# Kernel optimization log

Hardware: AMD Instinct MI355X
Metric: run time of the kernel (lower is better)

## Reference

```python
import jax, jax.numpy as jnp
import numpy as np

UNITS = 256
NUM_HEADS = 8
HEAD_DIM = UNITS // NUM_HEADS
B, N = 8, 2048


def setup_inputs() -> dict:
    key = jax.random.key(0)
    ks = jax.random.split(key, 7)
    node_features = jax.random.normal(ks[0], (B, N, UNITS), dtype=jnp.float32)
    adjacency_matrix = jax.random.randint(ks[1], (B, N, N), 0, 2, dtype=jnp.int32)
    # Glorot-ish scaled dense weights
    s = 1.0 / np.sqrt(UNITS)
    Wq = jax.random.normal(ks[2], (UNITS, UNITS), dtype=jnp.float32) * s
    Wk = jax.random.normal(ks[3], (UNITS, UNITS), dtype=jnp.float32) * s
    Wv = jax.random.normal(ks[4], (UNITS, UNITS), dtype=jnp.float32) * s
    Wo = jax.random.normal(ks[5], (UNITS, UNITS), dtype=jnp.float32) * s
    bo = jnp.zeros((UNITS,), dtype=jnp.float32)
    return {"node_features": node_features, "adjacency_matrix": adjacency_matrix,
            "Wq": Wq, "Wk": Wk, "Wv": Wv, "Wo": Wo, "bo": bo}


def reference(node_features, adjacency_matrix, Wq, Wk, Wv, Wo, bo):
    b, n, _ = node_features.shape
    h, d = NUM_HEADS, HEAD_DIM
    # projections -> [b, h, n, d]
    q = (node_features @ Wq).reshape(b, n, h, d).transpose(0, 2, 1, 3)
    k = (node_features @ Wk).reshape(b, n, h, d).transpose(0, 2, 1, 3)
    v = (node_features @ Wv).reshape(b, n, h, d).transpose(0, 2, 1, 3)
    scores = jnp.einsum('bhqd,bhkd->bhqk', q, k) / jnp.sqrt(jnp.float32(d))
    mask = adjacency_matrix[:, None, :, :] > 0  # [b,1,n,n] broadcasts over heads
    scores = jnp.where(mask, scores, jnp.float32(-1e9))
    w = jax.nn.softmax(scores, axis=-1)
    # dropout is identity at inference (training=None)
    ctx = jnp.einsum('bhqk,bhkd->bhqd', w, v)
    ctx = ctx.transpose(0, 2, 1, 3).reshape(b, n, h * d)
    return ctx @ Wo + bo
```

## Files before the change

kernel.cpp:

```cpp
#include <hip/hip_runtime.h>
#include <cstdint>
#include <cstddef>

#define B_ 8
#define N_ 2048
#define H_ 8
#define D_ 32
#define U_ 256

typedef _Float16 half8 __attribute__((ext_vector_type(8)));
typedef _Float16 half4 __attribute__((ext_vector_type(4)));
typedef float float4v __attribute__((ext_vector_type(4)));

__device__ __forceinline__ float fast_exp2(float x) {
#if __has_builtin(__builtin_amdgcn_exp2f)
  return __builtin_amdgcn_exp2f(x);
#else
  return exp2f(x);
#endif
}

__global__ __launch_bounds__(256)
void k_prep(const float* __restrict__ X,
            const float* __restrict__ Wq, const float* __restrict__ Wk,
            const float* __restrict__ Wv, const float* __restrict__ Wo,
            _Float16* __restrict__ Xh, _Float16* __restrict__ WT)
{
  __shared__ __attribute__((aligned(16))) float Ts[64][68];
  const int tid = threadIdx.x;
  const int bx = blockIdx.x;
  if (bx < 4) {
    const float* W = (bx == 0) ? Wq : (bx == 1) ? Wk : (bx == 2) ? Wv : Wo;
    const float scale = (bx == 0) ? 0.25505413f : 1.0f;
    _Float16* dstW = WT + (size_t)bx * (U_ * U_);
    const int r = tid >> 2, cs = tid & 3;
    for (int t = 0; t < 16; ++t) {
      const int k0 = (t >> 2) * 64, n0 = (t & 3) * 64;
#pragma unroll
      for (int j = 0; j < 4; ++j)
        *(float4v*)&Ts[r][cs * 16 + j * 4] =
            *(const float4v*)(W + (size_t)(k0 + r) * U_ + n0 + cs * 16 + j * 4);
      __syncthreads();
#pragma unroll
      for (int j = 0; j < 4; ++j) {
        half4 hv;
#pragma unroll
        for (int jj = 0; jj < 4; ++jj)
          hv[jj] = (_Float16)(Ts[cs * 16 + j * 4 + jj][r] * scale);
        *(half4*)(dstW + (size_t)(n0 + r) * U_ + k0 + cs * 16 + j * 4) = hv;
      }
      __syncthreads();
    }
  } else {
    const size_t base = ((size_t)(bx - 4) * 256 + tid) * 32;
#pragma unroll
    for (int i = 0; i < 4; ++i) {
      float4v a  = *(const float4v*)(X + base + i * 8);
      float4v b2 = *(const float4v*)(X + base + i * 8 + 4);
      half8 hv;
      hv[0] = (_Float16)a[0];  hv[1] = (_Float16)a[1];
      hv[2] = (_Float16)a[2];  hv[3] = (_Float16)a[3];
      hv[4] = (_Float16)b2[0]; hv[5] = (_Float16)b2[1];
      hv[6] = (_Float16)b2[2]; hv[7] = (_Float16)b2[3];
      *(half8*)(Xh + base + i * 8) = hv;
    }
  }
}

__global__ __launch_bounds__(256, 2)
void k_qkv2(const _Float16* __restrict__ Xh,
            const _Float16* __restrict__ WTq, const _Float16* __restrict__ WTk,
            const _Float16* __restrict__ WTv,
            _Float16* __restrict__ Qg, _Float16* __restrict__ Kg,
            _Float16* __restrict__ VTg)
{
  __shared__ __attribute__((aligned(16))) char qsmem[36864];
  _Float16* Xs = (_Float16*)qsmem;
  _Float16* Ws = (_Float16*)(qsmem + 18432);

  const int tid  = threadIdx.x;
  const int lane = tid & 63;
  const int w    = tid >> 6;
  const int c    = lane & 15;
  const int qd   = lane >> 4;

  const int bx   = blockIdx.x;
  const int proj = bx >> 1;
  const int nh   = bx & 1;
  const int n0l  = nh * 128;
  const int m0   = blockIdx.y * 128;
  const _Float16* WT = (proj == 0) ? WTq : ((proj == 1) ? WTk : WTv);

  const float4v zero4 = {0.f, 0.f, 0.f, 0.f};
  float4v acc[2][8];
#pragma unroll
  for (int i = 0; i < 2; ++i)
#pragma unroll
    for (int j = 0; j < 8; ++j) acc[i][j] = zero4;

  const int row = tid >> 1;
  const int off = (tid & 1) * 32;
  for (int kt = 0; kt < 4; ++kt) {
    const int k0 = kt * 64;
    {
      const _Float16* src = Xh + (size_t)(m0 + row) * U_ + k0 + off;
      _Float16* dst = &Xs[row * 72 + off];
#pragma unroll
      for (int i = 0; i < 4; ++i)
        *(half8*)(dst + i * 8) = *(const half8*)(src + i * 8);
    }
    {
      const _Float16* srcw = WT + (size_t)(n0l + row) * U_ + k0 + off;
      _Float16* dstw = &Ws[row * 72 + off];
#pragma unroll
      for (int i = 0; i < 4; ++i)
        *(half8*)(dstw + i * 8) = *(const half8*)(srcw + i * 8);
    }
    __syncthreads();
#pragma unroll
    for (int ks = 0; ks < 2; ++ks) {
      half8 af[2], bf[8];
#pragma unroll
      for (int mt = 0; mt < 2; ++mt)
        af[mt] = *(const half8*)&Xs[(w * 32 + mt * 16 + c) * 72 + ks * 32 + qd * 8];
#pragma unroll
      for (int nt = 0; nt < 8; ++nt)
        bf[nt] = *(const half8*)&Ws[(nt * 16 + c) * 72 + ks * 32 + qd * 8];
#pragma unroll
      for (int mt = 0; mt < 2; ++mt)
#pragma unroll
        for (int nt = 0; nt < 8; ++nt)
          acc[mt][nt] = __builtin_amdgcn_mfma_f32_16x16x32_f16(af[mt], bf[nt], acc[mt][nt], 0, 0, 0);
    }
    __syncthreads();
  }

  const int b   = m0 >> 11;
  const int nb0 = m0 & (N_ - 1);
  if (proj < 2) {
    _Float16* Og = (proj == 0) ? Qg : Kg;
#pragma unroll
    for (int mt = 0; mt < 2; ++mt)
#pragma unroll
      for (int nt = 0; nt < 8; ++nt)
#pragma unroll
        for (int r = 0; r < 4; ++r) {
          const int rowl = w * 32 + mt * 16 + qd * 4 + r;
          Og[(size_t)(b * N_ + nb0 + rowl) * U_ + n0l + nt * 16 + c] = (_Float16)acc[mt][nt][r];
        }
  } else {
    _Float16* tr = (_Float16*)qsmem;
#pragma unroll
    for (int mt = 0; mt < 2; ++mt)
#pragma unroll
      for (int nt = 0; nt < 8; ++nt)
#pragma unroll
        for (int r = 0; r < 4; ++r)
          tr[(nt * 16 + c) * 136 + w * 32 + mt * 16 + qd * 4 + r] = (_Float16)acc[mt][nt][r];
    __syncthreads();
    const int u = tid >> 1;
    const int seg = tid & 1;
    _Float16* dst = VTg + (size_t)(b * U_ + n0l + u) * N_ + nb0 + seg * 64;
#pragma unroll
    for (int i = 0; i < 8; ++i)
      *(half8*)(dst + i * 8) = *(const half8*)&tr[u * 136 + seg * 64 + i * 8];
  }
}

__global__ __launch_bounds__(256, 2)
void k_qkv(const float* __restrict__ X,
           const float* __restrict__ Wq, const float* __restrict__ Wk,
           const float* __restrict__ Wv,
           _Float16* __restrict__ Qg, _Float16* __restrict__ Kg,
           _Float16* __restrict__ VTg)
{
  __shared__ __attribute__((aligned(16))) char qsmem[36864];
  _Float16* Xs = (_Float16*)qsmem;
  _Float16* Ws = (_Float16*)(qsmem + 18432);

  const int tid  = threadIdx.x;
  const int lane = tid & 63;
  const int w    = tid >> 6;
  const int c    = lane & 15;
  const int qd   = lane >> 4;

  const int bx   = blockIdx.x;
  const int proj = bx >> 1;
  const int nh   = bx & 1;
  const int n0l  = nh * 128;
  const int m0   = blockIdx.y * 128;
  const float* Wp = (proj == 0) ? Wq : ((proj == 1) ? Wk : Wv);
  const float wscale = (proj == 0) ? 0.25505413f : 1.0f;

  const float4v zero4 = {0.f, 0.f, 0.f, 0.f};
  float4v acc[2][8];
#pragma unroll
  for (int i = 0; i < 2; ++i)
#pragma unroll
    for (int j = 0; j < 8; ++j) acc[i][j] = zero4;

  for (int kt = 0; kt < 4; ++kt) {
    const int k0 = kt * 64;
    {
      const int row = tid >> 1;
      const int off = (tid & 1) * 32;
      const float* src = X + (size_t)(m0 + row) * U_ + k0 + off;
      _Float16* dst = &Xs[row * 72 + off];
#pragma unroll
      for (int i = 0; i < 4; ++i) {
        float4v a  = *(const float4v*)(src + i * 8);
        float4v b2 = *(const float4v*)(src + i * 8 + 4);
        half8 hv;
        hv[0] = (_Float16)a[0];  hv[1] = (_Float16)a[1];
        hv[2] = (_Float16)a[2];  hv[3] = (_Float16)a[3];
        hv[4] = (_Float16)b2[0]; hv[5] = (_Float16)b2[1];
        hv[6] = (_Float16)b2[2]; hv[7] = (_Float16)b2[3];
        *(half8*)(dst + i * 8) = hv;
      }
    }
    {
      const int kl = tid & 63;
      const int ng = tid >> 6;
      const float* srcw = Wp + (size_t)(k0 + kl) * U_ + n0l + ng * 32;
#pragma unroll
      for (int j = 0; j < 8; ++j) {
        float4v a = *(const float4v*)(srcw + j * 4);
#pragma unroll
        for (int jj = 0; jj < 4; ++jj)
          Ws[(ng * 32 + j * 4 + jj) * 72 + kl] = (_Float16)(a[jj] * wscale);
      }
    }
    __syncthreads();
#pragma unroll
    for (int ks = 0; ks < 2; ++ks) {
      half8 af[2], bf[8];
#pragma unroll
      for (int mt = 0; mt < 2; ++mt)
        af[mt] = *(const half8*)&Xs[(w * 32 + mt * 16 + c) * 72 + ks * 32 + qd * 8];
#pragma unroll
      for (int nt = 0; nt < 8; ++nt)
        bf[nt] = *(const half8*)&Ws[(nt * 16 + c) * 72 + ks * 32 + qd * 8];
#pragma unroll
      for (int mt = 0; mt < 2; ++mt)
#pragma unroll
        for (int nt = 0; nt < 8; ++nt)
          acc[mt][nt] = __builtin_amdgcn_mfma_f32_16x16x32_f16(af[mt], bf[nt], acc[mt][nt], 0, 0, 0);
    }
    __syncthreads();
  }

  const int b   = m0 >> 11;
  const int nb0 = m0 & (N_ - 1);
  if (proj < 2) {
    _Float16* Og = (proj == 0) ? Qg : Kg;
#pragma unroll
    for (int mt = 0; mt < 2; ++mt)
#pragma unroll
      for (int nt = 0; nt < 8; ++nt)
#pragma unroll
        for (int r = 0; r < 4; ++r) {
          const int rowl = w * 32 + mt * 16 + qd * 4 + r;
          Og[(size_t)(b * N_ + nb0 + rowl) * U_ + n0l + nt * 16 + c] = (_Float16)acc[mt][nt][r];
        }
  } else {
    _Float16* tr = (_Float16*)qsmem;
#pragma unroll
    for (int mt = 0; mt < 2; ++mt)
#pragma unroll
      for (int nt = 0; nt < 8; ++nt)
#pragma unroll
        for (int r = 0; r < 4; ++r)
          tr[(nt * 16 + c) * 136 + w * 32 + mt * 16 + qd * 4 + r] = (_Float16)acc[mt][nt][r];
    __syncthreads();
    const int u = tid >> 1;
    const int seg = tid & 1;
    _Float16* dst = VTg + (size_t)(b * U_ + n0l + u) * N_ + nb0 + seg * 64;
#pragma unroll
    for (int i = 0; i < 8; ++i)
      *(half8*)(dst + i * 8) = *(const half8*)&tr[u * 136 + seg * 64 + i * 8];
  }
}

#define KS_H (32 * 264)
#define VT_H (256 * 40)

struct StageRegs {
  half8 k0, v0;
  int a0, a1;
};

__global__ __launch_bounds__(1024, 4)
void k_attn(const _Float16* __restrict__ Qg, const _Float16* __restrict__ Kg,
            const _Float16* __restrict__ VTg, const int* __restrict__ Adj,
            _Float16* __restrict__ Cg)
{
  __shared__ __attribute__((aligned(16))) _Float16 KsB[2][KS_H];
  __shared__ __attribute__((aligned(16))) _Float16 VTsB[2][VT_H];
  __shared__ __attribute__((aligned(8)))  unsigned int maskB[2][64];

  const int tid  = threadIdx.x;
  const int lane = tid & 63;
  const int w    = tid >> 6;
  const int h    = w & 7;
  const int qh   = w >> 3;
  const int c    = lane & 15;
  const int qd   = lane >> 4;
  const int wg   = blockIdx.x;
  const int b    = wg & 7;
  const int q0   = (wg >> 3) * 64;

  const _Float16* kptr = Kg + (size_t)(b * N_ + (tid >> 5)) * U_ + (tid & 31) * 8;
  const _Float16* vptr = VTg + (size_t)(b * U_ + (tid >> 2)) * N_ + (tid & 3) * 8;
  const int rr = lane >> 5;
  const int kk = lane & 31;
  const int* aptr = Adj + (size_t)(b * N_ + q0 + w * 4 + rr) * N_ + kk;

  half8 qb[2];
#pragma unroll
  for (int nt = 0; nt < 2; ++nt)
    qb[nt] = *(const half8*)(Qg + (size_t)(b * N_ + q0 + qh * 32 + nt * 16 + c) * U_ + h * D_ + qd * 8);

  const float4v init4 = {-8.f, -8.f, -8.f, -8.f};
  const float4v zero4 = {0.f, 0.f, 0.f, 0.f};
  float4v acc[2][2];
#pragma unroll
  for (int i = 0; i < 2; ++i)
#pragma unroll
    for (int j = 0; j < 2; ++j) acc[i][j] = zero4;
  float lrow[2] = {0.f, 0.f};

  auto load_tile = [&](int kt) -> StageRegs {
    StageRegs r;
    r.k0 = *(const half8*)(kptr + (size_t)kt * 32 * U_);
    r.v0 = *(const half8*)(vptr + (size_t)kt * 32);
    const int* as = aptr + (size_t)kt * 32;
    r.a0 = as[0];
    r.a1 = as[2 * N_];
    return r;
  };
  auto store_tile = [&](const StageRegs& r, int buf) {
    *(half8*)&KsB[buf][(tid >> 5) * 264 + (tid & 31) * 8] = r.k0;
    *(half8*)&VTsB[buf][(tid >> 2) * 40 + (tid & 3) * 8] = r.v0;
    unsigned long long bm;
    bm = __ballot(r.a0 > 0); if (lane == 0) *(unsigned long long*)&maskB[buf][w * 4 + 0] = bm;
    bm = __ballot(r.a1 > 0); if (lane == 0) *(unsigned long long*)&maskB[buf][w * 4 + 2] = bm;
  };
  auto compute_tile = [&](int buf) {
    half8 ka0 = *(const half8*)&KsB[buf][(0 * 16 + c) * 264 + h * D_ + qd * 8];
    half8 ka1 = *(const half8*)&KsB[buf][(1 * 16 + c) * 264 + h * D_ + qd * 8];
    half4 va[2][2];
#pragma unroll
    for (int mt = 0; mt < 2; ++mt)
#pragma unroll
      for (int kc = 0; kc < 2; ++kc)
        va[mt][kc] = *(const half4*)&VTsB[buf][(h * D_ + mt * 16 + c) * 40 + kc * 16 + qd * 4];
#pragma unroll
    for (int nt = 0; nt < 2; ++nt) {
      float4v s0 = __builtin_amdgcn_mfma_f32_16x16x32_f16(ka0, qb[nt], init4, 0, 0, 0);
      float4v s1 = __builtin_amdgcn_mfma_f32_16x16x32_f16(ka1, qb[nt], init4, 0, 0, 0);
      const unsigned int mq = maskB[buf][qh * 32 + nt * 16 + c];
      const unsigned int t0 = mq >> (qd * 4);
      const unsigned int t1 = mq >> (16 + qd * 4);
      half4 pb0, pb1;
      float ls = 0.f;
#pragma unroll
      for (int r = 0; r < 4; ++r) {
        float e0 = fast_exp2(s0[r]);
        float e1 = fast_exp2(s1[r]);
        float p0 = ((t0 >> r) & 1u) ? e0 : 0.f;
        float p1 = ((t1 >> r) & 1u) ? e1 : 0.f;
        ls += p0 + p1;
        pb0[r] = (_Float16)p0;
        pb1[r] = (_Float16)p1;
      }
      lrow[nt] += ls;
      acc[0][nt] = __builtin_amdgcn_mfma_f32_16x16x16f16(va[0][0], pb0, acc[0][nt], 0, 0, 0);
      acc[0][nt] = __builtin_amdgcn_mfma_f32_16x16x16f16(va[0][1], pb1, acc[0][nt], 0, 0, 0);
      acc[1][nt] = __builtin_amdgcn_mfma_f32_16x16x16f16(va[1][0], pb0, acc[1][nt], 0, 0, 0);
      acc[1][nt] = __builtin_amdgcn_mfma_f32_16x16x16f16(va[1][1], pb1, acc[1][nt], 0, 0, 0);
    }
  };

  StageRegs rA = load_tile(0);
  store_tile(rA, 0);
  StageRegs rB = load_tile(1);
  __syncthreads();

#pragma unroll 1
  for (int kt = 0; kt < 64; kt += 2) {
    if (kt + 2 < 64) rA = load_tile(kt + 2);
    compute_tile(0);
    store_tile(rB, 1);
    __syncthreads();
    if (kt + 3 < 64) rB = load_tile(kt + 3);
    compute_tile(1);
    if (kt + 2 < 64) store_tile(rA, 0);
    __syncthreads();
  }

  float rinv[2];
#pragma unroll
  for (int nt = 0; nt < 2; ++nt) {
    float l = lrow[nt];
    l += __shfl_xor(l, 16, 64);
    l += __shfl_xor(l, 32, 64);
    rinv[nt] = (l > 0.f) ? 1.f / l : 0.f;
  }
  _Float16* ctxS = (_Float16*)KsB;
#pragma unroll
  for (int mt = 0; mt < 2; ++mt)
#pragma unroll
    for (int nt = 0; nt < 2; ++nt) {
      half4 hv;
#pragma unroll
      for (int r = 0; r < 4; ++r)
        hv[r] = (_Float16)(acc[mt][nt][r] * rinv[nt]);
      *(half4*)&ctxS[(qh * 32 + nt * 16 + c) * 264 + h * D_ + mt * 16 + qd * 4] = hv;
    }
  __syncthreads();
  {
    const int row = tid >> 4;
    const int seg = tid & 15;
    _Float16* dst = Cg + (size_t)(b * N_ + q0 + row) * U_ + seg * 16;
    *(half8*)(dst + 0) = *(const half8*)&ctxS[row * 264 + seg * 16];
    *(half8*)(dst + 8) = *(const half8*)&ctxS[row * 264 + seg * 16 + 8];
  }
}

__global__ __launch_bounds__(256, 2)
void k_out2(const _Float16* __restrict__ Cg, const _Float16* __restrict__ WTo,
            const float* __restrict__ bo, float* __restrict__ Out)
{
  __shared__ __attribute__((aligned(16))) char osmem[36864];
  _Float16* Xs = (_Float16*)osmem;
  _Float16* Ws = (_Float16*)(osmem + 18432);

  const int tid  = threadIdx.x;
  const int lane = tid & 63;
  const int w    = tid >> 6;
  const int c    = lane & 15;
  const int qd   = lane >> 4;
  const int n0l  = blockIdx.x * 128;
  const int m0   = blockIdx.y * 128;

  const float4v zero4 = {0.f, 0.f, 0.f, 0.f};
  float4v acc[2][8];
#pragma unroll
  for (int i = 0; i < 2; ++i)
#pragma unroll
    for (int j = 0; j < 8; ++j) acc[i][j] = zero4;

  const int row = tid >> 1;
  const int off = (tid & 1) * 32;
  for (int kt = 0; kt < 4; ++kt) {
    const int k0 = kt * 64;
    {
      const _Float16* src = Cg + (size_t)(m0 + row) * U_ + k0 + off;
      _Float16* dst = &Xs[row * 72 + off];
#pragma unroll
      for (int i = 0; i < 4; ++i)
        *(half8*)(dst + i * 8) = *(const half8*)(src + i * 8);
    }
    {
      const _Float16* srcw = WTo + (size_t)(n0l + row) * U_ + k0 + off;
      _Float16* dstw = &Ws[row * 72 + off];
#pragma unroll
      for (int i = 0; i < 4; ++i)
        *(half8*)(dstw + i * 8) = *(const half8*)(srcw + i * 8);
    }
    __syncthreads();
#pragma unroll
    for (int ks = 0; ks < 2; ++ks) {
      half8 af[2], bf[8];
#pragma unroll
      for (int mt = 0; mt < 2; ++mt)
        af[mt] = *(const half8*)&Xs[(w * 32 + mt * 16 + c) * 72 + ks * 32 + qd * 8];
#pragma unroll
      for (int nt = 0; nt < 8; ++nt)
        bf[nt] = *(const half8*)&Ws[(nt * 16 + c) * 72 + ks * 32 + qd * 8];
#pragma unroll
      for (int mt = 0; mt < 2; ++mt)
#pragma unroll
        for (int nt = 0; nt < 8; ++nt)
          acc[mt][nt] = __builtin_amdgcn_mfma_f32_16x16x32_f16(af[mt], bf[nt], acc[mt][nt], 0, 0, 0);
    }
    __syncthreads();
  }

#pragma unroll
  for (int nt = 0; nt < 8; ++nt) {
    const float bias = bo[n0l + nt * 16 + c];
#pragma unroll
    for (int mt = 0; mt < 2; ++mt)
#pragma unroll
      for (int r = 0; r < 4; ++r) {
        const int rowl = w * 32 + mt * 16 + qd * 4 + r;
        Out[(size_t)(m0 + rowl) * U_ + n0l + nt * 16 + c] = acc[mt][nt][r] + bias;
      }
  }
}

__global__ __launch_bounds__(256, 2)
void k_out(const _Float16* __restrict__ Cg, const float* __restrict__ Wo,
           const float* __restrict__ bo, float* __restrict__ Out)
{
  __shared__ __attribute__((aligned(16))) char osmem[36864];
  _Float16* Xs = (_Float16*)osmem;
  _Float16* Ws = (_Float16*)(osmem + 18432);

  const int tid  = threadIdx.x;
  const int lane = tid & 63;
  const int w    = tid >> 6;
  const int c    = lane & 15;
  const int qd   = lane >> 4;
  const int n0l  = blockIdx.x * 128;
  const int m0   = blockIdx.y * 128;

  const float4v zero4 = {0.f, 0.f, 0.f, 0.f};
  float4v acc[2][8];
#pragma unroll
  for (int i = 0; i < 2; ++i)
#pragma unroll
    for (int j = 0; j < 8; ++j) acc[i][j] = zero4;

  for (int kt = 0; kt < 4; ++kt) {
    const int k0 = kt * 64;
    {
      const int row = tid >> 1;
      const int off = (tid & 1) * 32;
      const _Float16* src = Cg + (size_t)(m0 + row) * U_ + k0 + off;
      _Float16* dst = &Xs[row * 72 + off];
#pragma unroll
      for (int i = 0; i < 4; ++i)
        *(half8*)(dst + i * 8) = *(const half8*)(src + i * 8);
    }
    {
      const int kl = tid & 63;
      const int ng = tid >> 6;
      const float* srcw = Wo + (size_t)(k0 + kl) * U_ + n0l + ng * 32;
#pragma unroll
      for (int j = 0; j < 8; ++j) {
        float4v a = *(const float4v*)(srcw + j * 4);
#pragma unroll
        for (int jj = 0; jj < 4; ++jj)
          Ws[(ng * 32 + j * 4 + jj) * 72 + kl] = (_Float16)a[jj];
      }
    }
    __syncthreads();
#pragma unroll
    for (int ks = 0; ks < 2; ++ks) {
      half8 af[2], bf[8];
#pragma unroll
      for (int mt = 0; mt < 2; ++mt)
        af[mt] = *(const half8*)&Xs[(w * 32 + mt * 16 + c) * 72 + ks * 32 + qd * 8];
#pragma unroll
      for (int nt = 0; nt < 8; ++nt)
        bf[nt] = *(const half8*)&Ws[(nt * 16 + c) * 72 + ks * 32 + qd * 8];
#pragma unroll
      for (int mt = 0; mt < 2; ++mt)
#pragma unroll
        for (int nt = 0; nt < 8; ++nt)
          acc[mt][nt] = __builtin_amdgcn_mfma_f32_16x16x32_f16(af[mt], bf[nt], acc[mt][nt], 0, 0, 0);
    }
    __syncthreads();
  }

#pragma unroll
  for (int nt = 0; nt < 8; ++nt) {
    const float bias = bo[n0l + nt * 16 + c];
#pragma unroll
    for (int mt = 0; mt < 2; ++mt)
#pragma unroll
      for (int r = 0; r < 4; ++r) {
        const int rowl = w * 32 + mt * 16 + qd * 4 + r;
        Out[(size_t)(m0 + rowl) * U_ + n0l + nt * 16 + c] = acc[mt][nt][r] + bias;
      }
  }
}

extern "C" void kernel_launch(void* const* d_in, const int* in_sizes, int n_in,
                              void* d_out, int out_size, void* d_ws, size_t ws_size,
                              hipStream_t stream) {
  const float* X   = (const float*)d_in[0];
  const int*   Adj = (const int*)d_in[1];
  const float* Wq  = (const float*)d_in[2];
  const float* Wk  = (const float*)d_in[3];
  const float* Wv  = (const float*)d_in[4];
  const float* Wo  = (const float*)d_in[5];
  const float* bo  = (const float*)d_in[6];
  float* Out = (float*)d_out;

  const size_t elems = (size_t)B_ * N_ * U_;
  const size_t need  = (4 * elems + 4 * (size_t)(U_ * U_)) * sizeof(_Float16);

  if (ws_size >= need) {
    _Float16* A   = (_Float16*)d_ws;
    _Float16* Qg  = A + elems;
    _Float16* Kg  = Qg + elems;
    _Float16* VTg = Kg + elems;
    _Float16* WT  = VTg + elems;
    _Float16* WTq = WT;
    _Float16* WTk = WT + (size_t)U_ * U_;
    _Float16* WTv = WT + 2 * (size_t)U_ * U_;
    _Float16* WTo = WT + 3 * (size_t)U_ * U_;

    k_prep<<<dim3(516), 256, 0, stream>>>(X, Wq, Wk, Wv, Wo, A, WT);
    k_qkv2<<<dim3(6, 128), 256, 0, stream>>>(A, WTq, WTk, WTv, Qg, Kg, VTg);
    k_attn<<<dim3(256), 1024, 0, stream>>>(Qg, Kg, VTg, Adj, A );
    k_out2<<<dim3(2, 128), 256, 0, stream>>>(A , WTo, bo, Out);
  } else {
    _Float16* Qg  = (_Float16*)d_ws;
    _Float16* Kg  = Qg + elems;
    _Float16* VTg = Kg + elems;
    _Float16* Cg  = VTg + elems;

    k_qkv<<<dim3(6, 128), 256, 0, stream>>>(X, Wq, Wk, Wv, Qg, Kg, VTg);
    k_attn<<<dim3(256), 1024, 0, stream>>>(Qg, Kg, VTg, Adj, Cg);
    k_out<<<dim3(2, 128), 256, 0, stream>>>(Cg, Wo, bo, Out);
  }
}
```

Baseline: 339.6 us.

## Halve attention query tile per workgroup to 32 rows and double grid

The attention kernel now processes 32 query rows per 1024-thread workgroup instead of 64, so each wave handles one 16-row query tile rather than two, and the grid doubles to 512 workgroups. Launch bounds are raised so more waves can be resident with the lower register use. The aim is better load balance across the 256 compute units and higher occupancy. The cost is that K and V tiles are loaded from global memory and staged in shared memory twice as often per query, doubling K/V traffic and halving the MFMA work done per shared-memory load.

```diff
diff --git a/kernel.cpp b/kernel.cpp
--- a/kernel.cpp
+++ b/kernel.cpp
@@ -286,64 +286,54 @@
 
 struct StageRegs {
   half8 k0, v0;
-  int a0, a1;
+  int a0;
 };
 
-__global__ __launch_bounds__(1024, 4)
+__global__ __launch_bounds__(1024, 8)
 void k_attn(const _Float16* __restrict__ Qg, const _Float16* __restrict__ Kg,
             const _Float16* __restrict__ VTg, const int* __restrict__ Adj,
             _Float16* __restrict__ Cg)
 {
   __shared__ __attribute__((aligned(16))) _Float16 KsB[2][KS_H];
   __shared__ __attribute__((aligned(16))) _Float16 VTsB[2][VT_H];
-  __shared__ __attribute__((aligned(8)))  unsigned int maskB[2][64];
+  __shared__ __attribute__((aligned(8)))  unsigned int maskB[2][32];
 
   const int tid  = threadIdx.x;
   const int lane = tid & 63;
   const int w    = tid >> 6;
   const int h    = w & 7;
-  const int qh   = w >> 3;
+  const int qs   = w >> 3;
   const int c    = lane & 15;
   const int qd   = lane >> 4;
   const int wg   = blockIdx.x;
   const int b    = wg & 7;
-  const int q0   = (wg >> 3) * 64;
+  const int q0   = (wg >> 3) * 32;
 
   const _Float16* kptr = Kg + (size_t)(b * N_ + (tid >> 5)) * U_ + (tid & 31) * 8;
   const _Float16* vptr = VTg + (size_t)(b * U_ + (tid >> 2)) * N_ + (tid & 3) * 8;
   const int rr = lane >> 5;
   const int kk = lane & 31;
-  const int* aptr = Adj + (size_t)(b * N_ + q0 + w * 4 + rr) * N_ + kk;
-
-  half8 qb[2];
-#pragma unroll
-  for (int nt = 0; nt < 2; ++nt)
-    qb[nt] = *(const half8*)(Qg + (size_t)(b * N_ + q0 + qh * 32 + nt * 16 + c) * U_ + h * D_ + qd * 8);
+  const int* aptr = Adj + (size_t)(b * N_ + q0 + w * 2 + rr) * N_ + kk;
+
+  half8 qb = *(const half8*)(Qg + (size_t)(b * N_ + q0 + qs * 16 + c) * U_ + h * D_ + qd * 8);
 
   const float4v init4 = {-8.f, -8.f, -8.f, -8.f};
   const float4v zero4 = {0.f, 0.f, 0.f, 0.f};
-  float4v acc[2][2];
-#pragma unroll
-  for (int i = 0; i < 2; ++i)
-#pragma unroll
-    for (int j = 0; j < 2; ++j) acc[i][j] = zero4;
-  float lrow[2] = {0.f, 0.f};
+  float4v acc[2] = {zero4, zero4};
+  float lrow = 0.f;
 
   auto load_tile = [&](int kt) -> StageRegs {
     StageRegs r;
     r.k0 = *(const half8*)(kptr + (size_t)kt * 32 * U_);
     r.v0 = *(const half8*)(vptr + (size_t)kt * 32);
-    const int* as = aptr + (size_t)kt * 32;
-    r.a0 = as[0];
-    r.a1 = as[2 * N_];
+    r.a0 = *(aptr + (size_t)kt * 32);
     return r;
   };
   auto store_tile = [&](const StageRegs& r, int buf) {
     *(half8*)&KsB[buf][(tid >> 5) * 264 + (tid & 31) * 8] = r.k0;
     *(half8*)&VTsB[buf][(tid >> 2) * 40 + (tid & 3) * 8] = r.v0;
-    unsigned long long bm;
-    bm = __ballot(r.a0 > 0); if (lane == 0) *(unsigned long long*)&maskB[buf][w * 4 + 0] = bm;
-    bm = __ballot(r.a1 > 0); if (lane == 0) *(unsigned long long*)&maskB[buf][w * 4 + 2] = bm;
+    unsigned long long bm = __ballot(r.a0 > 0);
+    if (lane == 0) *(unsigned long long*)&maskB[buf][w * 2] = bm;
   };
   auto compute_tile = [&](int buf) {
     half8 ka0 = *(const half8*)&KsB[buf][(0 * 16 + c) * 264 + h * D_ + qd * 8];
@@ -354,31 +344,28 @@
 #pragma unroll
       for (int kc = 0; kc < 2; ++kc)
         va[mt][kc] = *(const half4*)&VTsB[buf][(h * D_ + mt * 16 + c) * 40 + kc * 16 + qd * 4];
-#pragma unroll
-    for (int nt = 0; nt < 2; ++nt) {
-      float4v s0 = __builtin_amdgcn_mfma_f32_16x16x32_f16(ka0, qb[nt], init4, 0, 0, 0);
-      float4v s1 = __builtin_amdgcn_mfma_f32_16x16x32_f16(ka1, qb[nt], init4, 0, 0, 0);
-      const unsigned int mq = maskB[buf][qh * 32 + nt * 16 + c];
-      const unsigned int t0 = mq >> (qd * 4);
-      const unsigned int t1 = mq >> (16 + qd * 4);
-      half4 pb0, pb1;
-      float ls = 0.f;
-#pragma unroll
-      for (int r = 0; r < 4; ++r) {
-        float e0 = fast_exp2(s0[r]);
-        float e1 = fast_exp2(s1[r]);
-        float p0 = ((t0 >> r) & 1u) ? e0 : 0.f;
-        float p1 = ((t1 >> r) & 1u) ? e1 : 0.f;
-        ls += p0 + p1;
-        pb0[r] = (_Float16)p0;
-        pb1[r] = (_Float16)p1;
-      }
-      lrow[nt] += ls;
-      acc[0][nt] = __builtin_amdgcn_mfma_f32_16x16x16f16(va[0][0], pb0, acc[0][nt], 0, 0, 0);
-      acc[0][nt] = __builtin_amdgcn_mfma_f32_16x16x16f16(va[0][1], pb1, acc[0][nt], 0, 0, 0);
-      acc[1][nt] = __builtin_amdgcn_mfma_f32_16x16x16f16(va[1][0], pb0, acc[1][nt], 0, 0, 0);
-      acc[1][nt] = __builtin_amdgcn_mfma_f32_16x16x16f16(va[1][1], pb1, acc[1][nt], 0, 0, 0);
-    }
+    float4v s0 = __builtin_amdgcn_mfma_f32_16x16x32_f16(ka0, qb, init4, 0, 0, 0);
+    float4v s1 = __builtin_amdgcn_mfma_f32_16x16x32_f16(ka1, qb, init4, 0, 0, 0);
+    const unsigned int mq = maskB[buf][qs * 16 + c];
+    const unsigned int t0 = mq >> (qd * 4);
+    const unsigned int t1 = mq >> (16 + qd * 4);
+    half4 pb0, pb1;
+    float ls = 0.f;
+#pragma unroll
+    for (int r = 0; r < 4; ++r) {
+      float e0 = fast_exp2(s0[r]);
+      float e1 = fast_exp2(s1[r]);
+      float p0 = ((t0 >> r) & 1u) ? e0 : 0.f;
+      float p1 = ((t1 >> r) & 1u) ? e1 : 0.f;
+      ls += p0 + p1;
+      pb0[r] = (_Float16)p0;
+      pb1[r] = (_Float16)p1;
+    }
+    lrow += ls;
+    acc[0] = __builtin_amdgcn_mfma_f32_16x16x16f16(va[0][0], pb0, acc[0], 0, 0, 0);
+    acc[0] = __builtin_amdgcn_mfma_f32_16x16x16f16(va[0][1], pb1, acc[0], 0, 0, 0);
+    acc[1] = __builtin_amdgcn_mfma_f32_16x16x16f16(va[1][0], pb0, acc[1], 0, 0, 0);
+    acc[1] = __builtin_amdgcn_mfma_f32_16x16x16f16(va[1][1], pb1, acc[1], 0, 0, 0);
   };
 
   StageRegs rA = load_tile(0);
@@ -398,32 +385,26 @@
     __syncthreads();
   }
 
-  float rinv[2];
-#pragma unroll
-  for (int nt = 0; nt < 2; ++nt) {
-    float l = lrow[nt];
-    l += __shfl_xor(l, 16, 64);
-    l += __shfl_xor(l, 32, 64);
-    rinv[nt] = (l > 0.f) ? 1.f / l : 0.f;
-  }
+  float l = lrow;
+  l += __shfl_xor(l, 16, 64);
+  l += __shfl_xor(l, 32, 64);
+  const float rinv = (l > 0.f) ? 1.f / l : 0.f;
+
   _Float16* ctxS = (_Float16*)KsB;
 #pragma unroll
-  for (int mt = 0; mt < 2; ++mt)
-#pragma unroll
-    for (int nt = 0; nt < 2; ++nt) {
-      half4 hv;
-#pragma unroll
-      for (int r = 0; r < 4; ++r)
-        hv[r] = (_Float16)(acc[mt][nt][r] * rinv[nt]);
-      *(half4*)&ctxS[(qh * 32 + nt * 16 + c) * 264 + h * D_ + mt * 16 + qd * 4] = hv;
-    }
+  for (int mt = 0; mt < 2; ++mt) {
+    half4 hv;
+#pragma unroll
+    for (int r = 0; r < 4; ++r)
+      hv[r] = (_Float16)(acc[mt][r] * rinv);
+    *(half4*)&ctxS[(qs * 16 + c) * 264 + h * D_ + mt * 16 + qd * 4] = hv;
+  }
   __syncthreads();
   {
-    const int row = tid >> 4;
-    const int seg = tid & 15;
-    _Float16* dst = Cg + (size_t)(b * N_ + q0 + row) * U_ + seg * 16;
-    *(half8*)(dst + 0) = *(const half8*)&ctxS[row * 264 + seg * 16];
-    *(half8*)(dst + 8) = *(const half8*)&ctxS[row * 264 + seg * 16 + 8];
+    const int row = tid >> 5;
+    const int seg = tid & 31;
+    _Float16* dst = Cg + (size_t)(b * N_ + q0 + row) * U_ + seg * 8;
+    *(half8*)dst = *(const half8*)&ctxS[row * 264 + seg * 8];
   }
 }
 
@@ -606,7 +587,7 @@
 
     k_prep<<<dim3(516), 256, 0, stream>>>(X, Wq, Wk, Wv, Wo, A, WT);
     k_qkv2<<<dim3(6, 128), 256, 0, stream>>>(A, WTq, WTk, WTv, Qg, Kg, VTg);
-    k_attn<<<dim3(256), 1024, 0, stream>>>(Qg, Kg, VTg, Adj, A );
+    k_attn<<<dim3(512), 1024, 0, stream>>>(Qg, Kg, VTg, Adj, A );
     k_out2<<<dim3(2, 128), 256, 0, stream>>>(A , WTo, bo, Out);
   } else {
     _Float16* Qg  = (_Float16*)d_ws;
@@ -615,7 +596,7 @@
     _Float16* Cg  = VTg + elems;
 
     k_qkv<<<dim3(6, 128), 256, 0, stream>>>(X, Wq, Wk, Wv, Qg, Kg, VTg);
-    k_attn<<<dim3(256), 1024, 0, stream>>>(Qg, Kg, VTg, Adj, Cg);
+    k_attn<<<dim3(512), 1024, 0, stream>>>(Qg, Kg, VTg, Adj, Cg);
     k_out<<<dim3(2, 128), 256, 0, stream>>>(Cg, Wo, bo, Out);
   }
 }
```

Result: slower. 614.4 us (+80.9%).

## Halve per-block query/row tiles in attention and projection GEMMs to double grid size

Applied to the files above, without the earlier changes.

The attention kernel now runs 512-thread blocks, each covering 32 queries across all 8 heads, and launches 512 blocks instead of 256. Staging loads are widened so fewer threads still fill the shared K/V tiles. The QKV and output GEMMs shrink their M tile from 128 to 64 rows and launch twice as many blocks. The aim is better occupancy and CU balance, at the cost of more K/V and Adj tile reloads per query and less reuse per block.

```diff
diff --git a/kernel.cpp b/kernel.cpp
--- a/kernel.cpp
+++ b/kernel.cpp
@@ -74,9 +74,9 @@
             _Float16* __restrict__ Qg, _Float16* __restrict__ Kg,
             _Float16* __restrict__ VTg)
 {
-  __shared__ __attribute__((aligned(16))) char qsmem[36864];
+  __shared__ __attribute__((aligned(16))) char qsmem[27648];
   _Float16* Xs = (_Float16*)qsmem;
-  _Float16* Ws = (_Float16*)(qsmem + 18432);
+  _Float16* Ws = (_Float16*)(qsmem + 9216);
 
   const int tid  = threadIdx.x;
   const int lane = tid & 63;
@@ -88,30 +88,27 @@
   const int proj = bx >> 1;
   const int nh   = bx & 1;
   const int n0l  = nh * 128;
-  const int m0   = blockIdx.y * 128;
+  const int m0   = blockIdx.y * 64;
   const _Float16* WT = (proj == 0) ? WTq : ((proj == 1) ? WTk : WTv);
 
   const float4v zero4 = {0.f, 0.f, 0.f, 0.f};
-  float4v acc[2][8];
-#pragma unroll
-  for (int i = 0; i < 2; ++i)
-#pragma unroll
-    for (int j = 0; j < 8; ++j) acc[i][j] = zero4;
-
-  const int row = tid >> 1;
-  const int off = (tid & 1) * 32;
+  float4v acc[8];
+#pragma unroll
+  for (int j = 0; j < 8; ++j) acc[j] = zero4;
+
+  const int xrow = tid >> 2, xoff = (tid & 3) * 16;
+  const int wrow = tid >> 1, woff = (tid & 1) * 32;
   for (int kt = 0; kt < 4; ++kt) {
     const int k0 = kt * 64;
     {
-      const _Float16* src = Xh + (size_t)(m0 + row) * U_ + k0 + off;
-      _Float16* dst = &Xs[row * 72 + off];
-#pragma unroll
-      for (int i = 0; i < 4; ++i)
-        *(half8*)(dst + i * 8) = *(const half8*)(src + i * 8);
-    }
-    {
-      const _Float16* srcw = WT + (size_t)(n0l + row) * U_ + k0 + off;
-      _Float16* dstw = &Ws[row * 72 + off];
+      const _Float16* src = Xh + (size_t)(m0 + xrow) * U_ + k0 + xoff;
+      _Float16* dst = &Xs[xrow * 72 + xoff];
+      *(half8*)(dst)     = *(const half8*)(src);
+      *(half8*)(dst + 8) = *(const half8*)(src + 8);
+    }
+    {
+      const _Float16* srcw = WT + (size_t)(n0l + wrow) * U_ + k0 + woff;
+      _Float16* dstw = &Ws[wrow * 72 + woff];
 #pragma unroll
       for (int i = 0; i < 4; ++i)
         *(half8*)(dstw + i * 8) = *(const half8*)(srcw + i * 8);
@@ -119,18 +116,14 @@
     __syncthreads();
 #pragma unroll
     for (int ks = 0; ks < 2; ++ks) {
-      half8 af[2], bf[8];
-#pragma unroll
-      for (int mt = 0; mt < 2; ++mt)
-        af[mt] = *(const half8*)&Xs[(w * 32 + mt * 16 + c) * 72 + ks * 32 + qd * 8];
+      half8 af = *(const half8*)&Xs[(w * 16 + c) * 72 + ks * 32 + qd * 8];
+      half8 bf[8];
 #pragma unroll
       for (int nt = 0; nt < 8; ++nt)
         bf[nt] = *(const half8*)&Ws[(nt * 16 + c) * 72 + ks * 32 + qd * 8];
 #pragma unroll
-      for (int mt = 0; mt < 2; ++mt)
-#pragma unroll
-        for (int nt = 0; nt < 8; ++nt)
-          acc[mt][nt] = __builtin_amdgcn_mfma_f32_16x16x32_f16(af[mt], bf[nt], acc[mt][nt], 0, 0, 0);
+      for (int nt = 0; nt < 8; ++nt)
+        acc[nt] = __builtin_amdgcn_mfma_f32_16x16x32_f16(af, bf[nt], acc[nt], 0, 0, 0);
     }
     __syncthreads();
   }
@@ -140,30 +133,26 @@
   if (proj < 2) {
     _Float16* Og = (proj == 0) ? Qg : Kg;
 #pragma unroll
-    for (int mt = 0; mt < 2; ++mt)
-#pragma unroll
-      for (int nt = 0; nt < 8; ++nt)
-#pragma unroll
-        for (int r = 0; r < 4; ++r) {
-          const int rowl = w * 32 + mt * 16 + qd * 4 + r;
-          Og[(size_t)(b * N_ + nb0 + rowl) * U_ + n0l + nt * 16 + c] = (_Float16)acc[mt][nt][r];
-        }
+    for (int nt = 0; nt < 8; ++nt)
+#pragma unroll
+      for (int r = 0; r < 4; ++r) {
+        const int rowl = w * 16 + qd * 4 + r;
+        Og[(size_t)(b * N_ + nb0 + rowl) * U_ + n0l + nt * 16 + c] = (_Float16)acc[nt][r];
+      }
   } else {
     _Float16* tr = (_Float16*)qsmem;
 #pragma unroll
-    for (int mt = 0; mt < 2; ++mt)
-#pragma unroll
-      for (int nt = 0; nt < 8; ++nt)
-#pragma unroll
-        for (int r = 0; r < 4; ++r)
-          tr[(nt * 16 + c) * 136 + w * 32 + mt * 16 + qd * 4 + r] = (_Float16)acc[mt][nt][r];
+    for (int nt = 0; nt < 8; ++nt)
+#pragma unroll
+      for (int r = 0; r < 4; ++r)
+        tr[(nt * 16 + c) * 72 + w * 16 + qd * 4 + r] = (_Float16)acc[nt][r];
     __syncthreads();
     const int u = tid >> 1;
     const int seg = tid & 1;
-    _Float16* dst = VTg + (size_t)(b * U_ + n0l + u) * N_ + nb0 + seg * 64;
-#pragma unroll
-    for (int i = 0; i < 8; ++i)
-      *(half8*)(dst + i * 8) = *(const half8*)&tr[u * 136 + seg * 64 + i * 8];
+    _Float16* dst = VTg + (size_t)(b * U_ + n0l + u) * N_ + nb0 + seg * 32;
+#pragma unroll
+    for (int i = 0; i < 4; ++i)
+      *(half8*)(dst + i * 8) = *(const half8*)&tr[u * 72 + seg * 32 + i * 8];
   }
 }
 
@@ -285,32 +274,30 @@
 #define VT_H (256 * 40)
 
 struct StageRegs {
-  half8 k0, v0;
+  half8 k0, k1, v0, v1;
   int a0, a1;
 };
 
-__global__ __launch_bounds__(1024, 4)
+__global__ __launch_bounds__(512, 2)
 void k_attn(const _Float16* __restrict__ Qg, const _Float16* __restrict__ Kg,
             const _Float16* __restrict__ VTg, const int* __restrict__ Adj,
             _Float16* __restrict__ Cg)
 {
   __shared__ __attribute__((aligned(16))) _Float16 KsB[2][KS_H];
   __shared__ __attribute__((aligned(16))) _Float16 VTsB[2][VT_H];
-  __shared__ __attribute__((aligned(8)))  unsigned int maskB[2][64];
+  __shared__ __attribute__((aligned(8)))  unsigned int maskB[2][32];
 
   const int tid  = threadIdx.x;
   const int lane = tid & 63;
   const int w    = tid >> 6;
-  const int h    = w & 7;
-  const int qh   = w >> 3;
   const int c    = lane & 15;
   const int qd   = lane >> 4;
   const int wg   = blockIdx.x;
   const int b    = wg & 7;
-  const int q0   = (wg >> 3) * 64;
-
-  const _Float16* kptr = Kg + (size_t)(b * N_ + (tid >> 5)) * U_ + (tid & 31) * 8;
-  const _Float16* vptr = VTg + (size_t)(b * U_ + (tid >> 2)) * N_ + (tid & 3) * 8;
+  const int q0   = (wg >> 3) * 32;
+
+  const _Float16* kptr = Kg + (size_t)(b * N_ + (tid >> 4)) * U_ + (tid & 15) * 16;
+  const _Float16* vptr = VTg + (size_t)(b * U_ + (tid >> 1)) * N_ + (tid & 1) * 16;
   const int rr = lane >> 5;
   const int kk = lane & 31;
   const int* aptr = Adj + (size_t)(b * N_ + q0 + w * 4 + rr) * N_ + kk;
@@ -318,7 +305,7 @@
   half8 qb[2];
 #pragma unroll
   for (int nt = 0; nt < 2; ++nt)
-    qb[nt] = *(const half8*)(Qg + (size_t)(b * N_ + q0 + qh * 32 + nt * 16 + c) * U_ + h * D_ + qd * 8);
+    qb[nt] = *(const half8*)(Qg + (size_t)(b * N_ + q0 + nt * 16 + c) * U_ + w * D_ + qd * 8);
 
   const float4v init4 = {-8.f, -8.f, -8.f, -8.f};
   const float4v zero4 = {0.f, 0.f, 0.f, 0.f};
@@ -331,34 +318,38 @@
 
   auto load_tile = [&](int kt) -> StageRegs {
     StageRegs r;
-    r.k0 = *(const half8*)(kptr + (size_t)kt * 32 * U_);
-    r.v0 = *(const half8*)(vptr + (size_t)kt * 32);
+    const _Float16* ks = kptr + (size_t)kt * 32 * U_;
+    const _Float16* vs = vptr + (size_t)kt * 32;
     const int* as = aptr + (size_t)kt * 32;
+    r.k0 = *(const half8*)ks;  r.k1 = *(const half8*)(ks + 8);
+    r.v0 = *(const half8*)vs;  r.v1 = *(const half8*)(vs + 8);
     r.a0 = as[0];
     r.a1 = as[2 * N_];
     return r;
   };
   auto store_tile = [&](const StageRegs& r, int buf) {
-    *(half8*)&KsB[buf][(tid >> 5) * 264 + (tid & 31) * 8] = r.k0;
-    *(half8*)&VTsB[buf][(tid >> 2) * 40 + (tid & 3) * 8] = r.v0;
+    _Float16* kd = &KsB[buf][(tid >> 4) * 264 + (tid & 15) * 16];
+    *(half8*)kd = r.k0;  *(half8*)(kd + 8) = r.k1;
+    _Float16* vd = &VTsB[buf][(tid >> 1) * 40 + (tid & 1) * 16];
+    *(half8*)vd = r.v0;  *(half8*)(vd + 8) = r.v1;
     unsigned long long bm;
     bm = __ballot(r.a0 > 0); if (lane == 0) *(unsigned long long*)&maskB[buf][w * 4 + 0] = bm;
     bm = __ballot(r.a1 > 0); if (lane == 0) *(unsigned long long*)&maskB[buf][w * 4 + 2] = bm;
   };
   auto compute_tile = [&](int buf) {
-    half8 ka0 = *(const half8*)&KsB[buf][(0 * 16 + c) * 264 + h * D_ + qd * 8];
-    half8 ka1 = *(const half8*)&KsB[buf][(1 * 16 + c) * 264 + h * D_ + qd * 8];
+    half8 ka0 = *(const half8*)&KsB[buf][(0 * 16 + c) * 264 + w * D_ + qd * 8];
+    half8 ka1 = *(const half8*)&KsB[buf][(1 * 16 + c) * 264 + w * D_ + qd * 8];
     half4 va[2][2];
 #pragma unroll
     for (int mt = 0; mt < 2; ++mt)
 #pragma unroll
       for (int kc = 0; kc < 2; ++kc)
-        va[mt][kc] = *(const half4*)&VTsB[buf][(h * D_ + mt * 16 + c) * 40 + kc * 16 + qd * 4];
+        va[mt][kc] = *(const half4*)&VTsB[buf][(w * D_ + mt * 16 + c) * 40 + kc * 16 + qd * 4];
 #pragma unroll
     for (int nt = 0; nt < 2; ++nt) {
       float4v s0 = __builtin_amdgcn_mfma_f32_16x16x32_f16(ka0, qb[nt], init4, 0, 0, 0);
       float4v s1 = __builtin_amdgcn_mfma_f32_16x16x32_f16(ka1, qb[nt], init4, 0, 0, 0);
-      const unsigned int mq = maskB[buf][qh * 32 + nt * 16 + c];
+      const unsigned int mq = maskB[buf][nt * 16 + c];
       const unsigned int t0 = mq >> (qd * 4);
       const unsigned int t1 = mq >> (16 + qd * 4);
       half4 pb0, pb1;
@@ -415,7 +406,7 @@
 #pragma unroll
       for (int r = 0; r < 4; ++r)
         hv[r] = (_Float16)(acc[mt][nt][r] * rinv[nt]);
-      *(half4*)&ctxS[(qh * 32 + nt * 16 + c) * 264 + h * D_ + mt * 16 + qd * 4] = hv;
+      *(half4*)&ctxS[(nt * 16 + c) * 264 + w * D_ + mt * 16 + qd * 4] = hv;
     }
   __syncthreads();
   {
@@ -431,9 +422,9 @@
 void k_out2(const _Float16* __restrict__ Cg, const _Float16* __restrict__ WTo,
             const float* __restrict__ bo, float* __restrict__ Out)
 {
-  __shared__ __attribute__((aligned(16))) char osmem[36864];
+  __shared__ __attribute__((aligned(16))) char osmem[27648];
   _Float16* Xs = (_Float16*)osmem;
-  _Float16* Ws = (_Float16*)(osmem + 18432);
+  _Float16* Ws = (_Float16*)(osmem + 9216);
 
   const int tid  = threadIdx.x;
   const int lane = tid & 63;
@@ -441,29 +432,26 @@
   const int c    = lane & 15;
   const int qd   = lane >> 4;
   const int n0l  = blockIdx.x * 128;
-  const int m0   = blockIdx.y * 128;
+  const int m0   = blockIdx.y * 64;
 
   const float4v zero4 = {0.f, 0.f, 0.f, 0.f};
-  float4v acc[2][8];
-#pragma unroll
-  for (int i = 0; i < 2; ++i)
-#pragma unroll
-    for (int j = 0; j < 8; ++j) acc[i][j] = zero4;
-
-  const int row = tid >> 1;
-  const int off = (tid & 1) * 32;
+  float4v acc[8];
+#pragma unroll
+  for (int j = 0; j < 8; ++j) acc[j] = zero4;
+
+  const int xrow = tid >> 2, xoff = (tid & 3) * 16;
+  const int wrow = tid >> 1, woff = (tid & 1) * 32;
   for (int kt = 0; kt < 4; ++kt) {
     const int k0 = kt * 64;
     {
-      const _Float16* src = Cg + (size_t)(m0 + row) * U_ + k0 + off;
-      _Float16* dst = &Xs[row * 72 + off];
-#pragma unroll
-      for (int i = 0; i < 4; ++i)
-        *(half8*)(dst + i * 8) = *(const half8*)(src + i * 8);
-    }
-    {
-      const _Float16* srcw = WTo + (size_t)(n0l + row) * U_ + k0 + off;
-      _Float16* dstw = &Ws[row * 72 + off];
+      const _Float16* src = Cg + (size_t)(m0 + xrow) * U_ + k0 + xoff;
+      _Float16* dst = &Xs[xrow * 72 + xoff];
+      *(half8*)(dst)     = *(const half8*)(src);
+      *(half8*)(dst + 8) = *(const half8*)(src + 8);
+    }
+    {
+      const _Float16* srcw = WTo + (size_t)(n0l + wrow) * U_ + k0 + woff;
+      _Float16* dstw = &Ws[wrow * 72 + woff];
 #pragma unroll
       for (int i = 0; i < 4; ++i)
         *(half8*)(dstw + i * 8) = *(const half8*)(srcw + i * 8);
@@ -471,18 +459,14 @@
     __syncthreads();
 #pragma unroll
     for (int ks = 0; ks < 2; ++ks) {
-      half8 af[2], bf[8];
-#pragma unroll
-      for (int mt = 0; mt < 2; ++mt)
-        af[mt] = *(const half8*)&Xs[(w * 32 + mt * 16 + c) * 72 + ks * 32 + qd * 8];
+      half8 af = *(const half8*)&Xs[(w * 16 + c) * 72 + ks * 32 + qd * 8];
+      half8 bf[8];
 #pragma unroll
       for (int nt = 0; nt < 8; ++nt)
         bf[nt] = *(const half8*)&Ws[(nt * 16 + c) * 72 + ks * 32 + qd * 8];
 #pragma unroll
-      for (int mt = 0; mt < 2; ++mt)
-#pragma unroll
-        for (int nt = 0; nt < 8; ++nt)
-          acc[mt][nt] = __builtin_amdgcn_mfma_f32_16x16x32_f16(af[mt], bf[nt], acc[mt][nt], 0, 0, 0);
+      for (int nt = 0; nt < 8; ++nt)
+        acc[nt] = __builtin_amdgcn_mfma_f32_16x16x32_f16(af, bf[nt], acc[nt], 0, 0, 0);
     }
     __syncthreads();
   }
@@ -491,12 +475,10 @@
   for (int nt = 0; nt < 8; ++nt) {
     const float bias = bo[n0l + nt * 16 + c];
 #pragma unroll
-    for (int mt = 0; mt < 2; ++mt)
-#pragma unroll
-      for (int r = 0; r < 4; ++r) {
-        const int rowl = w * 32 + mt * 16 + qd * 4 + r;
-        Out[(size_t)(m0 + rowl) * U_ + n0l + nt * 16 + c] = acc[mt][nt][r] + bias;
-      }
+    for (int r = 0; r < 4; ++r) {
+      const int rowl = w * 16 + qd * 4 + r;
+      Out[(size_t)(m0 + rowl) * U_ + n0l + nt * 16 + c] = acc[nt][r] + bias;
+    }
   }
 }
 
@@ -605,9 +587,9 @@
     _Float16* WTo = WT + 3 * (size_t)U_ * U_;
 
     k_prep<<<dim3(516), 256, 0, stream>>>(X, Wq, Wk, Wv, Wo, A, WT);
-    k_qkv2<<<dim3(6, 128), 256, 0, stream>>>(A, WTq, WTk, WTv, Qg, Kg, VTg);
-    k_attn<<<dim3(256), 1024, 0, stream>>>(Qg, Kg, VTg, Adj, A );
-    k_out2<<<dim3(2, 128), 256, 0, stream>>>(A , WTo, bo, Out);
+    k_qkv2<<<dim3(6, 256), 256, 0, stream>>>(A, WTq, WTk, WTv, Qg, Kg, VTg);
+    k_attn<<<dim3(512), 512, 0, stream>>>(Qg, Kg, VTg, Adj, A );
+    k_out2<<<dim3(2, 256), 256, 0, stream>>>(A , WTo, bo, Out);
   } else {
     _Float16* Qg  = (_Float16*)d_ws;
     _Float16* Kg  = Qg + elems;
@@ -615,7 +597,7 @@
     _Float16* Cg  = VTg + elems;
 
     k_qkv<<<dim3(6, 128), 256, 0, stream>>>(X, Wq, Wk, Wv, Qg, Kg, VTg);
-    k_attn<<<dim3(256), 1024, 0, stream>>>(Qg, Kg, VTg, Adj, Cg);
+    k_attn<<<dim3(512), 512, 0, stream>>>(Qg, Kg, VTg, Adj, Cg);
     k_out<<<dim3(2, 128), 256, 0, stream>>>(Cg, Wo, bo, Out);
   }
 }
```

After: 393.5 us. +15.9%, slower.
